# Optimization experiments

Measured on AMD Instinct MI355X. Metric: run time of the kernel, lower is better.

The kernel has to match this reference:

```python
import jax, jax.numpy as jnp
import numpy as np

N_NODES = 50000
N_EDGES = 800000
IN_CH, HID, OUT_CH, EDGE_DIM = 256, 128, 64, 64
NUM_LAYERS = 3


def _linear_init(key, fan_in, fan_out):
    # torch nn.Linear default: U(-1/sqrt(fan_in), 1/sqrt(fan_in))
    kw, kb = jax.random.split(key)
    bound = 1.0 / np.sqrt(fan_in)
    W = jax.random.uniform(kw, (fan_in, fan_out), minval=-bound, maxval=bound, dtype=jnp.float32)
    b = jax.random.uniform(kb, (fan_out,), minval=-bound, maxval=bound, dtype=jnp.float32)
    return W, b


def setup_inputs() -> dict:
    key = jax.random.key(0)
    ks = jax.random.split(key, 8)
    x = jax.random.normal(ks[0], (N_NODES, IN_CH), dtype=jnp.float32)
    edge_index = jax.random.randint(ks[1], (2, N_EDGES), 0, N_NODES, dtype=jnp.int64)
    edge_attr = jax.random.normal(ks[2], (N_EDGES, EDGE_DIM), dtype=jnp.float32)
    W_in, b_in = _linear_init(ks[3], IN_CH, HID)
    W_e, b_e = _linear_init(ks[4], EDGE_DIM, HID)
    W1, b1 = _linear_init(ks[5], HID, HID)
    W2, b2 = _linear_init(ks[6], HID, HID)
    W_out, b_out = _linear_init(ks[7], HID, OUT_CH)
    return {"x": x, "edge_index": edge_index, "edge_attr": edge_attr,
            "W_in": W_in, "b_in": b_in, "W_e": W_e, "b_e": b_e,
            "W1": W1, "b1": b1, "W2": W2, "b2": b2,
            "W_out": W_out, "b_out": b_out}


def reference(x, edge_index, edge_attr, W_in, b_in, W_e, b_e, W1, b1, W2, b2, W_out, b_out):
    N = x.shape[0]
    src, dst = edge_index[0], edge_index[1]
    # input projection (in_channels != hidden_channels)
    h = x @ W_in + b_in                      # [N, HID]
    # edge projection is layer-independent (shared GINEConv weights)
    e = edge_attr @ W_e + b_e                # [E, HID]
    for _ in range(NUM_LAYERS):
        # GINEConv: message = relu(h_src + e), sum-aggregate to dst, eps=0
        msg = jax.nn.relu(h[src] + e)        # [E, HID]
        agg = jax.ops.segment_sum(msg, dst, num_segments=N)
        z = h + agg                          # (1+eps)*h + agg, eps=0
        # conv nn: MLP Linear->relu->Linear (plain_last)
        z = jax.nn.relu(z @ W1 + b1) @ W2 + b2
        # outer act
        h = jax.nn.relu(z)
    return h @ W_out + b_out                 # [N, OUT_CH]
```

## Files before the change

kernel.cpp:

```cpp
#include <hip/hip_runtime.h>
#include <hip/hip_bf16.h>
#include <stdint.h>

#define N_NODES 50000
#define N_EDGES 800000
#define IN_CH 256
#define HID 128
#define OUT_CH 64
#define EDGE_DIM 64

#define AGG_EW  64
#define AGG_CAP 128
#define AGG_B   (N_EDGES / AGG_EW)
#define SCB     196

typedef __hip_bfloat16 bf16;
typedef __attribute__((ext_vector_type(8))) short short8;
typedef __attribute__((ext_vector_type(4))) float f32x4;

__device__ __forceinline__ void st_out(float* p, float v) { *p = v; }
__device__ __forceinline__ void st_out(bf16* p, float v) { *p = __float2bfloat16(v); }

__device__ __forceinline__ void wt_one(const float* W, bf16* Wt, int K, int N, int i) {
    int n = i % N, k = i / N;
    Wt[n * K + k] = __float2bfloat16(W[i]);
}
__launch_bounds__(256)
__global__ void wt_prep_all(const float* W_in, const float* W_e, const float* W1,
                            const float* W2, const float* W_out,
                            bf16* Wt_in, bf16* Wt_e, bf16* Wt_1, bf16* Wt_2, bf16* Wt_out) {
    int i = blockIdx.x * 256 + threadIdx.x;
    if (i < 32768)       wt_one(W_in,  Wt_in,  256, 128, i);
    else if (i < 40960)  wt_one(W_e,   Wt_e,    64, 128, i - 32768);
    else if (i < 57344)  wt_one(W1,    Wt_1,   128, 128, i - 40960);
    else if (i < 73728)  wt_one(W2,    Wt_2,   128, 128, i - 57344);
    else if (i < 81920)  wt_one(W_out, Wt_out, 128,  64, i - 73728);
}

template<int KTOT, int N, int MROWS, bool RELU, typename InT, typename OutT>
__launch_bounds__(256)
__global__ void gemm_mfma(const InT* __restrict__ A, const bf16* __restrict__ Wt,
                          const float* __restrict__ b, OutT* __restrict__ out, int M) {
    static_assert(KTOT % 64 == 0, "");
    constexpr int KC  = 64;
    constexpr int NCH = KTOT / KC;
    constexpr int KCP = KC + 8;
    constexpr int NT  = N / 16;
    constexpr int MT  = MROWS / 64;
    __shared__ __align__(16) bf16 Ws[N * KCP];
    __shared__ __align__(16) bf16 As[MROWS * KCP];

    const int tid  = threadIdx.x;
    const int wave = tid >> 6;
    const int lane = tid & 63;
    const int quad = lane >> 4;
    const int l16  = lane & 15;
    const int base = blockIdx.x * MROWS;

    f32x4 acc[MT][NT];
    #pragma unroll
    for (int m = 0; m < MT; m++)
        #pragma unroll
        for (int i = 0; i < NT; i++) acc[m][i] = (f32x4){0.f, 0.f, 0.f, 0.f};

    for (int ch = 0; ch < NCH; ch++) {
        const int kc = ch * KC;
        constexpr int WIT = N * KC / (256 * 8);
        #pragma unroll
        for (int it = 0; it < WIT; it++) {
            int t8 = (it * 256 + tid) * 8;
            int n = t8 / KC, k = t8 % KC;
            *(uint4*)&Ws[n * KCP + k] = *(const uint4*)&Wt[n * KTOT + kc + k];
        }
        if constexpr (sizeof(InT) == 4) {
            constexpr int AIT = MROWS * KC / (256 * 4);
            #pragma unroll
            for (int it = 0; it < AIT; it++) {
                int t4 = (it * 256 + tid) * 4;
                int r = t4 / KC, k = t4 % KC;
                int gr = base + r;
                float4 v = (gr < M) ? *(const float4*)&A[(size_t)gr * KTOT + kc + k]
                                    : make_float4(0.f, 0.f, 0.f, 0.f);
                *(__hip_bfloat162*)&As[r * KCP + k]     = __float22bfloat162_rn(make_float2(v.x, v.y));
                *(__hip_bfloat162*)&As[r * KCP + k + 2] = __float22bfloat162_rn(make_float2(v.z, v.w));
            }
        } else {
            constexpr int AIT = MROWS * KC / (256 * 8);
            #pragma unroll
            for (int it = 0; it < AIT; it++) {
                int t8 = (it * 256 + tid) * 8;
                int r = t8 / KC, k = t8 % KC;
                int gr = base + r;
                uint4 v = (gr < M) ? *(const uint4*)&A[(size_t)gr * KTOT + kc + k]
                                   : make_uint4(0u, 0u, 0u, 0u);
                *(uint4*)&As[r * KCP + k] = v;
            }
        }
        __syncthreads();

        #pragma unroll
        for (int ks = 0; ks < KC / 32; ks++) {
            short8 af[MT];
            #pragma unroll
            for (int m = 0; m < MT; m++)
                af[m] = *(const short8*)&As[(wave * MT * 16 + m * 16 + l16) * KCP + ks * 32 + quad * 8];
            #pragma unroll
            for (int nt = 0; nt < NT; nt++) {
                short8 bfr = *(const short8*)&Ws[(nt * 16 + l16) * KCP + ks * 32 + quad * 8];
                #pragma unroll
                for (int m = 0; m < MT; m++)
                    acc[m][nt] = __builtin_amdgcn_mfma_f32_16x16x32_bf16(af[m], bfr, acc[m][nt], 0, 0, 0);
            }
        }
        __syncthreads();
    }

    #pragma unroll
    for (int m = 0; m < MT; m++) {
        const int r0 = base + wave * MT * 16 + m * 16 + quad * 4;
        #pragma unroll
        for (int reg = 0; reg < 4; reg++) {
            int gr = r0 + reg;
            if (gr < M) {
                #pragma unroll
                for (int nt = 0; nt < NT; nt++) {
                    int col = nt * 16 + l16;
                    float v = acc[m][nt][reg] + b[col];
                    if (RELU) v = fmaxf(v, 0.f);
                    st_out(&out[(size_t)gr * N + col], v);
                }
            }
        }
    }
}

__launch_bounds__(256)
__global__ void hist_kernel(const int* __restrict__ ei, int* __restrict__ counts) {
    int edge = blockIdx.x * 256 + threadIdx.x;
    if (edge < N_EDGES) atomicAdd(&counts[ei[N_EDGES + edge]], 1);
}

__launch_bounds__(256)
__global__ void scan_a(const int* __restrict__ counts, int* __restrict__ bsum) {
    __shared__ int sh[256];
    const int tid = threadIdx.x;
    int n = blockIdx.x * 256 + tid;
    sh[tid] = (n < N_NODES) ? counts[n] : 0;
    __syncthreads();
    for (int off = 128; off > 0; off >>= 1) {
        if (tid < off) sh[tid] += sh[tid + off];
        __syncthreads();
    }
    if (tid == 0) bsum[blockIdx.x] = sh[0];
}

__launch_bounds__(256)
__global__ void scan_b(const int* __restrict__ bsum, int* __restrict__ bpre) {
    __shared__ int sh[256];
    const int tid = threadIdx.x;
    int v = (tid < SCB) ? bsum[tid] : 0;
    sh[tid] = v;
    __syncthreads();
    for (int off = 1; off < 256; off <<= 1) {
        int t = (tid >= off) ? sh[tid - off] : 0;
        __syncthreads();
        sh[tid] += t;
        __syncthreads();
    }
    if (tid < SCB) bpre[tid] = sh[tid] - v;
}

__launch_bounds__(256)
__global__ void scan_c(const int* __restrict__ counts, const int* __restrict__ bpre,
                       int* __restrict__ offsets, int* __restrict__ cursor) {
    __shared__ int sh[256];
    const int tid = threadIdx.x;
    int n = blockIdx.x * 256 + tid;
    int c = (n < N_NODES) ? counts[n] : 0;
    sh[tid] = c;
    __syncthreads();
    for (int off = 1; off < 256; off <<= 1) {
        int t = (tid >= off) ? sh[tid - off] : 0;
        __syncthreads();
        sh[tid] += t;
        __syncthreads();
    }
    if (n < N_NODES) {
        int excl = bpre[blockIdx.x] + sh[tid] - c;
        offsets[n] = excl;
        cursor[n]  = excl;
    }
    if (blockIdx.x == 0 && tid == 0) offsets[N_NODES] = N_EDGES;
}

__launch_bounds__(256)
__global__ void scan_d(const int* __restrict__ offsets, int* __restrict__ blkstart) {
    int n = blockIdx.x * 256 + threadIdx.x;
    if (n > N_NODES) return;
    int v = (n == N_NODES) ? N_EDGES : offsets[n];
    int lo = 0;
    if (n > 0) lo = offsets[n - 1] / AGG_EW + 1;
    int hi = v / AGG_EW;
    for (int bb = lo; bb <= hi; bb++) blkstart[bb] = n;
    if (n == N_NODES) blkstart[AGG_B + 1] = N_NODES;
}

__launch_bounds__(256)
__global__ void scatter_perm(const int* __restrict__ ei, int* __restrict__ cursor,
                             int* __restrict__ poe, int* __restrict__ srcs) {
    int edge = blockIdx.x * 256 + threadIdx.x;
    if (edge >= N_EDGES) return;
    int dst = ei[N_EDGES + edge];
    int pos = atomicAdd(&cursor[dst], 1);
    poe[edge] = pos;
    srcs[pos] = ei[edge];
}

__launch_bounds__(256)
__global__ void ea_permute(const float* __restrict__ ea, const int* __restrict__ poe,
                           bf16* __restrict__ eas) {
    int t = blockIdx.x * 256 + threadIdx.x;
    int edge = t >> 4, l16 = t & 15;
    if (edge >= N_EDGES) return;
    float4 v = *(const float4*)&ea[(size_t)edge * EDGE_DIM + l16 * 4];
    int pos = poe[edge];
    __hip_bfloat162 p0 = __float22bfloat162_rn(make_float2(v.x, v.y));
    __hip_bfloat162 p1 = __float22bfloat162_rn(make_float2(v.z, v.w));
    uint2 u = make_uint2(*(uint32_t*)&p0, *(uint32_t*)&p1);
    *(uint2*)&eas[(size_t)pos * EDGE_DIM + l16 * 4] = u;
}

__device__ __forceinline__ float blo(uint32_t u) { return __uint_as_float(u << 16); }
__device__ __forceinline__ float bhi(uint32_t u) { return __uint_as_float(u & 0xffff0000u); }

__launch_bounds__(256)
__global__ void agg_fused(const int* __restrict__ offsets, const int* __restrict__ blkstart,
                          const int* __restrict__ srcs, const bf16* __restrict__ eas,
                          const bf16* __restrict__ Wt_e, const float* __restrict__ b_e,
                          const bf16* __restrict__ h, bf16* __restrict__ z) {
    constexpr int P = 136;
    __shared__ __align__(16) bf16 et[AGG_CAP * P];
    __shared__ int srcs_s[AGG_CAP + 4];

    const int b    = blockIdx.x;
    const int tid  = threadIdx.x;
    const int wave = tid >> 6;
    const int lane = tid & 63;
    const int quad = lane >> 4;
    const int l16  = lane & 15;

    const int n0 = blkstart[b], n1 = blkstart[b + 1];
    if (n0 >= n1) return;
    const int e0 = offsets[n0];
    int e1 = offsets[n1];
    if (e1 > e0 + AGG_CAP) e1 = e0 + AGG_CAP;
    const int ne = e1 - e0;

    if (tid < AGG_CAP + 4) srcs_s[tid] = (tid < ne) ? srcs[e0 + tid] : 0;

    short8 af[2][2];
    float4 bias[2];
    #pragma unroll
    for (int ct = 0; ct < 2; ct++) {
        int chr = (wave * 2 + ct) * 16 + l16;
        #pragma unroll
        for (int ks = 0; ks < 2; ks++)
            af[ct][ks] = *(const short8*)&Wt_e[chr * EDGE_DIM + ks * 32 + quad * 8];
        bias[ct] = *(const float4*)&b_e[(wave * 2 + ct) * 16 + quad * 4];
    }
    const int nsub = (ne + 15) >> 4;
    short8 cb0 = (short8){0,0,0,0,0,0,0,0}, cb1 = cb0;
    if (l16 < ne) {
        cb0 = *(const short8*)&eas[(size_t)(e0 + l16) * EDGE_DIM + quad * 8];
        cb1 = *(const short8*)&eas[(size_t)(e0 + l16) * EDGE_DIM + 32 + quad * 8];
    }
    for (int es = 0; es < nsub; es++) {
        short8 nb0 = (short8){0,0,0,0,0,0,0,0}, nb1 = nb0;
        int nrow = (es + 1) * 16 + l16;
        if (nrow < ne) {
            nb0 = *(const short8*)&eas[(size_t)(e0 + nrow) * EDGE_DIM + quad * 8];
            nb1 = *(const short8*)&eas[(size_t)(e0 + nrow) * EDGE_DIM + 32 + quad * 8];
        }
        #pragma unroll
        for (int ct = 0; ct < 2; ct++) {
            f32x4 acc = (f32x4){0.f, 0.f, 0.f, 0.f};
            acc = __builtin_amdgcn_mfma_f32_16x16x32_bf16(af[ct][0], cb0, acc, 0, 0, 0);
            acc = __builtin_amdgcn_mfma_f32_16x16x32_bf16(af[ct][1], cb1, acc, 0, 0, 0);
            int row = es * 16 + l16;
            int ch0 = (wave * 2 + ct) * 16 + quad * 4;
            __hip_bfloat162 p0 = __float22bfloat162_rn(make_float2(acc[0] + bias[ct].x, acc[1] + bias[ct].y));
            __hip_bfloat162 p1 = __float22bfloat162_rn(make_float2(acc[2] + bias[ct].z, acc[3] + bias[ct].w));
            *(uint2*)&et[row * P + ch0] = make_uint2(*(uint32_t*)&p0, *(uint32_t*)&p1);
        }
        cb0 = nb0; cb1 = nb1;
    }
    __syncthreads();

    const int c8 = l16 * 8;
    for (int n = n0 + wave; n < n1; n += 4) {
        int s  = offsets[n] - e0;
        int ee = offsets[n + 1] - e0;
        if (ee > ne) ee = ne;
        float a[8];
        #pragma unroll
        for (int j = 0; j < 8; j++) a[j] = 0.f;
        for (int i = s; i < ee; i += 4) {
            int idx = i + quad;
            if (idx < ee) {
                int src = srcs_s[idx];
                uint4 hv = *(const uint4*)&h[(size_t)src * HID + c8];
                uint4 ev = *(const uint4*)&et[idx * P + c8];
                uint32_t hs[4] = {hv.x, hv.y, hv.z, hv.w};
                uint32_t vs[4] = {ev.x, ev.y, ev.z, ev.w};
                #pragma unroll
                for (int j = 0; j < 4; j++) {
                    a[2 * j]     += fmaxf(blo(hs[j]) + blo(vs[j]), 0.f);
                    a[2 * j + 1] += fmaxf(bhi(hs[j]) + bhi(vs[j]), 0.f);
                }
            }
        }
        #pragma unroll
        for (int j = 0; j < 8; j++) {
            a[j] += __shfl_xor(a[j], 16);
            a[j] += __shfl_xor(a[j], 32);
        }
        if (lane < 16) {
            uint4 hn = *(const uint4*)&h[(size_t)n * HID + c8];
            uint32_t hs[4] = {hn.x, hn.y, hn.z, hn.w};
            uint32_t o[4];
            #pragma unroll
            for (int j = 0; j < 4; j++) {
                __hip_bfloat162 p = __float22bfloat162_rn(
                    make_float2(a[2 * j] + blo(hs[j]), a[2 * j + 1] + bhi(hs[j])));
                o[j] = *(uint32_t*)&p;
            }
            *(uint4*)&z[(size_t)n * HID + c8] = make_uint4(o[0], o[1], o[2], o[3]);
        }
    }
}

extern "C" void kernel_launch(void* const* d_in, const int* in_sizes, int n_in,
                              void* d_out, int out_size, void* d_ws, size_t ws_size,
                              hipStream_t stream) {
    const float* x     = (const float*)d_in[0];
    const int*   ei    = (const int*)d_in[1];
    const float* ea    = (const float*)d_in[2];
    const float* W_in  = (const float*)d_in[3];
    const float* b_in  = (const float*)d_in[4];
    const float* W_e   = (const float*)d_in[5];
    const float* b_e   = (const float*)d_in[6];
    const float* W1    = (const float*)d_in[7];
    const float* b1    = (const float*)d_in[8];
    const float* W2    = (const float*)d_in[9];
    const float* b2    = (const float*)d_in[10];
    const float* W_out = (const float*)d_in[11];
    const float* b_out = (const float*)d_in[12];
    float* out = (float*)d_out;

    char* ws = (char*)d_ws;
    size_t off = 0;
    bf16*  h        = (bf16*) (ws + off); off += (size_t)N_NODES * HID * 2;
    bf16*  z        = (bf16*) (ws + off); off += (size_t)N_NODES * HID * 2;
    bf16*  eas      = (bf16*) (ws + off); off += (size_t)N_EDGES * EDGE_DIM * 2;
    int*   counts   = (int*)  (ws + off); off += (size_t)N_NODES * 4;
    int*   offsets  = (int*)  (ws + off); off += (size_t)(N_NODES + 1) * 4;
    int*   cursor   = (int*)  (ws + off); off += (size_t)N_NODES * 4;
    int*   poe      = (int*)  (ws + off); off += (size_t)N_EDGES * 4;
    int*   srcs     = (int*)  (ws + off); off += (size_t)N_EDGES * 4;
    int*   blkstart = (int*)  (ws + off); off += (size_t)(AGG_B + 2) * 4;
    int*   bsum     = (int*)  (ws + off); off += (size_t)SCB * 4;
    int*   bpre     = (int*)  (ws + off); off += (size_t)SCB * 4;
    bf16*  Wt_in    = (bf16*) (ws + off); off += (size_t)HID * IN_CH * 2;
    bf16*  Wt_e     = (bf16*) (ws + off); off += (size_t)HID * EDGE_DIM * 2;
    bf16*  Wt_1     = (bf16*) (ws + off); off += (size_t)HID * HID * 2;
    bf16*  Wt_2     = (bf16*) (ws + off); off += (size_t)HID * HID * 2;
    bf16*  Wt_out   = (bf16*) (ws + off); off += (size_t)OUT_CH * HID * 2;

    wt_prep_all<<<(81920 + 255) / 256, 256, 0, stream>>>(
        W_in, W_e, W1, W2, W_out, Wt_in, Wt_e, Wt_1, Wt_2, Wt_out);

    hipMemsetAsync(counts, 0, (size_t)N_NODES * 4, stream);
    hist_kernel<<<(N_EDGES + 255) / 256, 256, 0, stream>>>(ei, counts);
    scan_a<<<SCB, 256, 0, stream>>>(counts, bsum);
    scan_b<<<1, 256, 0, stream>>>(bsum, bpre);
    scan_c<<<SCB, 256, 0, stream>>>(counts, bpre, offsets, cursor);
    scan_d<<<SCB, 256, 0, stream>>>(offsets, blkstart);
    scatter_perm<<<(N_EDGES + 255) / 256, 256, 0, stream>>>(ei, cursor, poe, srcs);

    ea_permute<<<(N_EDGES * 16 + 255) / 256, 256, 0, stream>>>(ea, poe, eas);

    gemm_mfma<IN_CH, HID, 64, false, float, bf16>
        <<<(N_NODES + 63) / 64, 256, 0, stream>>>(x, Wt_in, b_in, h, N_NODES);

    for (int layer = 0; layer < 3; ++layer) {
        agg_fused<<<AGG_B + 1, 256, 0, stream>>>(offsets, blkstart, srcs, eas, Wt_e, b_e, h, z);
        gemm_mfma<HID, HID, 64, true, bf16, bf16>
            <<<(N_NODES + 63) / 64, 256, 0, stream>>>(z, Wt_1, b1, h, N_NODES);
        gemm_mfma<HID, HID, 64, true, bf16, bf16>
            <<<(N_NODES + 63) / 64, 256, 0, stream>>>(h, Wt_2, b2, z, N_NODES);
        bf16* t = h; h = z; z = t;
    }

    gemm_mfma<HID, OUT_CH, 64, false, bf16, float>
        <<<(N_NODES + 63) / 64, 256, 0, stream>>>(h, Wt_out, b_out, out, N_NODES);
}
```

Measured before the change: 902.9 us.

## Prefetch gathered source rows before edge GEMM and precompute block metadata

```diff
diff --git a/kernel.cpp b/kernel.cpp
--- a/kernel.cpp
+++ b/kernel.cpp
@@ -206,6 +206,18 @@
 }
 
 __launch_bounds__(256)
+__global__ void scan_e(const int* __restrict__ blkstart, const int* __restrict__ offsets,
+                       int4* __restrict__ blkmeta) {
+    int b = blockIdx.x * 256 + threadIdx.x;
+    if (b > AGG_B) return;
+    int n0 = blkstart[b], n1 = blkstart[b + 1];
+    int e0 = offsets[n0];
+    int e1 = offsets[n1];
+    if (e1 > e0 + AGG_CAP) e1 = e0 + AGG_CAP;
+    blkmeta[b] = make_int4(n0, n1, e0, e1);
+}
+
+__launch_bounds__(256)
 __global__ void scatter_perm(const int* __restrict__ ei, int* __restrict__ cursor,
                              int* __restrict__ poe, int* __restrict__ srcs) {
     int edge = blockIdx.x * 256 + threadIdx.x;
@@ -234,13 +246,12 @@
 __device__ __forceinline__ float bhi(uint32_t u) { return __uint_as_float(u & 0xffff0000u); }
 
 __launch_bounds__(256)
-__global__ void agg_fused(const int* __restrict__ offsets, const int* __restrict__ blkstart,
+__global__ void agg_fused(const int* __restrict__ offsets, const int4* __restrict__ blkmeta,
                           const int* __restrict__ srcs, const bf16* __restrict__ eas,
                           const bf16* __restrict__ Wt_e, const float* __restrict__ b_e,
                           const bf16* __restrict__ h, bf16* __restrict__ z) {
     constexpr int P = 136;
     __shared__ __align__(16) bf16 et[AGG_CAP * P];
-    __shared__ int srcs_s[AGG_CAP + 4];
 
     const int b    = blockIdx.x;
     const int tid  = threadIdx.x;
@@ -249,14 +260,27 @@
     const int quad = lane >> 4;
     const int l16  = lane & 15;
 
-    const int n0 = blkstart[b], n1 = blkstart[b + 1];
+    const int4 mt = blkmeta[b];
+    const int n0 = mt.x, n1 = mt.y, e0 = mt.z, e1 = mt.w;
     if (n0 >= n1) return;
-    const int e0 = offsets[n0];
-    int e1 = offsets[n1];
-    if (e1 > e0 + AGG_CAP) e1 = e0 + AGG_CAP;
     const int ne = e1 - e0;
-
-    if (tid < AGG_CAP + 4) srcs_s[tid] = (tid < ne) ? srcs[e0 + tid] : 0;
+    const int c8 = l16 * 8;
+
+    int sv[2][4];
+    #pragma unroll
+    for (int r = 0; r < 2; r++)
+        #pragma unroll
+        for (int j = 0; j < 4; j++) {
+            int pos = e0 + r * 64 + wave * 16 + j * 4 + quad;
+            if (pos >= N_EDGES) pos = N_EDGES - 1;
+            sv[r][j] = srcs[pos];
+        }
+    uint4 hv[2][4];
+    #pragma unroll
+    for (int r = 0; r < 2; r++)
+        #pragma unroll
+        for (int j = 0; j < 4; j++)
+            hv[r][j] = *(const uint4*)&h[(size_t)sv[r][j] * HID + c8];
 
     short8 af[2][2];
     float4 bias[2];
@@ -296,26 +320,45 @@
     }
     __syncthreads();
 
-    const int c8 = l16 * 8;
+    #pragma unroll
+    for (int r = 0; r < 2; r++)
+        #pragma unroll
+        for (int j = 0; j < 4; j++) {
+            int idx = r * 64 + wave * 16 + j * 4 + quad;
+            if (idx < ne) {
+                uint4 ev = *(const uint4*)&et[idx * P + c8];
+                uint32_t hs[4] = {hv[r][j].x, hv[r][j].y, hv[r][j].z, hv[r][j].w};
+                uint32_t vs[4] = {ev.x, ev.y, ev.z, ev.w};
+                uint32_t o[4];
+                #pragma unroll
+                for (int k = 0; k < 4; k++) {
+                    float lo = fmaxf(blo(hs[k]) + blo(vs[k]), 0.f);
+                    float hi = fmaxf(bhi(hs[k]) + bhi(vs[k]), 0.f);
+                    __hip_bfloat162 p = __float22bfloat162_rn(make_float2(lo, hi));
+                    o[k] = *(uint32_t*)&p;
+                }
+                *(uint4*)&et[idx * P + c8] = make_uint4(o[0], o[1], o[2], o[3]);
+            }
+        }
+    __syncthreads();
+
     for (int n = n0 + wave; n < n1; n += 4) {
-        int s  = offsets[n] - e0;
+        int s  = offsets[n]     - e0;
         int ee = offsets[n + 1] - e0;
         if (ee > ne) ee = ne;
+        uint4 hn = *(const uint4*)&h[(size_t)n * HID + c8];
         float a[8];
         #pragma unroll
         for (int j = 0; j < 8; j++) a[j] = 0.f;
         for (int i = s; i < ee; i += 4) {
             int idx = i + quad;
             if (idx < ee) {
-                int src = srcs_s[idx];
-                uint4 hv = *(const uint4*)&h[(size_t)src * HID + c8];
-                uint4 ev = *(const uint4*)&et[idx * P + c8];
-                uint32_t hs[4] = {hv.x, hv.y, hv.z, hv.w};
-                uint32_t vs[4] = {ev.x, ev.y, ev.z, ev.w};
+                uint4 mv = *(const uint4*)&et[idx * P + c8];
+                uint32_t ms[4] = {mv.x, mv.y, mv.z, mv.w};
                 #pragma unroll
                 for (int j = 0; j < 4; j++) {
-                    a[2 * j]     += fmaxf(blo(hs[j]) + blo(vs[j]), 0.f);
-                    a[2 * j + 1] += fmaxf(bhi(hs[j]) + bhi(vs[j]), 0.f);
+                    a[2 * j]     += blo(ms[j]);
+                    a[2 * j + 1] += bhi(ms[j]);
                 }
             }
         }
@@ -325,7 +368,6 @@
             a[j] += __shfl_xor(a[j], 32);
         }
         if (lane < 16) {
-            uint4 hn = *(const uint4*)&h[(size_t)n * HID + c8];
             uint32_t hs[4] = {hn.x, hn.y, hn.z, hn.w};
             uint32_t o[4];
             #pragma unroll
@@ -370,6 +412,8 @@
     int*   blkstart = (int*)  (ws + off); off += (size_t)(AGG_B + 2) * 4;
     int*   bsum     = (int*)  (ws + off); off += (size_t)SCB * 4;
     int*   bpre     = (int*)  (ws + off); off += (size_t)SCB * 4;
+    off = (off + 15) & ~(size_t)15;
+    int4*  blkmeta  = (int4*) (ws + off); off += (size_t)(AGG_B + 1) * 16;
     bf16*  Wt_in    = (bf16*) (ws + off); off += (size_t)HID * IN_CH * 2;
     bf16*  Wt_e     = (bf16*) (ws + off); off += (size_t)HID * EDGE_DIM * 2;
     bf16*  Wt_1     = (bf16*) (ws + off); off += (size_t)HID * HID * 2;
@@ -385,6 +429,7 @@
     scan_b<<<1, 256, 0, stream>>>(bsum, bpre);
     scan_c<<<SCB, 256, 0, stream>>>(counts, bpre, offsets, cursor);
     scan_d<<<SCB, 256, 0, stream>>>(offsets, blkstart);
+    scan_e<<<(AGG_B + 256) / 256, 256, 0, stream>>>(blkstart, offsets, blkmeta);
     scatter_perm<<<(N_EDGES + 255) / 256, 256, 0, stream>>>(ei, cursor, poe, srcs);
 
     ea_permute<<<(N_EDGES * 16 + 255) / 256, 256, 0, stream>>>(ea, poe, eas);
@@ -393,7 +438,7 @@
         <<<(N_NODES + 63) / 64, 256, 0, stream>>>(x, Wt_in, b_in, h, N_NODES);
 
     for (int layer = 0; layer < 3; ++layer) {
-        agg_fused<<<AGG_B + 1, 256, 0, stream>>>(offsets, blkstart, srcs, eas, Wt_e, b_e, h, z);
+        agg_fused<<<AGG_B + 1, 256, 0, stream>>>(offsets, blkmeta, srcs, eas, Wt_e, b_e, h, z);
         gemm_mfma<HID, HID, 64, true, bf16, bf16>
             <<<(N_NODES + 63) / 64, 256, 0, stream>>>(z, Wt_1, b1, h, N_NODES);
         gemm_mfma<HID, HID, 64, true, bf16, bf16>
```

Result: faster. 862.2 us (-4.5%).
